# Kernel tuning notes

Measured on AMD Instinct MI355X. Metric: run time of the kernel, lower is better.

The kernel has to match this reference:

```python
import jax, jax.numpy as jnp
import numpy as np

N_NODES = 50000
N_EDGES = 1600000
IN_DIM = 128
HID = 128
N_GRAPHS = 64
N_CLASSES = 1


def _seg_sum(x, ids, n):
    return jax.ops.segment_sum(x, ids, num_segments=n)


def _gcn_layer(h, W, b, src, dst, src_isqrt, dst_isqrt):
    # DGL GraphConv, norm='both': D_dst^{-1/2} A D_src^{-1/2} (h W) + b
    hw = h @ W                                  # [N, out]
    msg = (hw * src_isqrt[:, None])[src]        # gather -> [E, out]
    agg = _seg_sum(msg, dst, h.shape[0])        # scatter-add -> [N, out]
    return agg * dst_isqrt[:, None] + b


def setup_inputs() -> dict:
    key = jax.random.key(0)
    ks = jax.random.split(key, 16)
    x = jax.random.normal(ks[0], (N_NODES, IN_DIM), dtype=jnp.float32)
    src = jax.random.randint(ks[1], (N_EDGES,), 0, N_NODES)
    dst = jax.random.randint(ks[2], (N_EDGES,), 0, N_NODES)
    graph_id = jnp.sort(jax.random.randint(ks[3], (N_NODES,), 0, N_GRAPHS))
    s = 1.0 / np.sqrt(HID)
    params = {
        'W1': jax.random.uniform(ks[4], (IN_DIM, HID), jnp.float32, -s, s),
        'b1': jnp.zeros((HID,), jnp.float32),
        'W2': jax.random.uniform(ks[5], (HID, HID), jnp.float32, -s, s),
        'b2': jnp.zeros((HID,), jnp.float32),
        'Wc1': jax.random.uniform(ks[6], (HID, HID // 2), jnp.float32, -s, s),
        'bc1': jnp.zeros((HID // 2,), jnp.float32),
        'Wc2': jax.random.uniform(ks[7], (HID // 2, HID // 4), jnp.float32, -s, s),
        'bc2': jnp.zeros((HID // 4,), jnp.float32),
        'Wc3': jax.random.uniform(ks[8], (HID // 4, HID // 8), jnp.float32, -s, s),
        'bc3': jnp.zeros((HID // 8,), jnp.float32),
        'Wc4': jax.random.uniform(ks[9], (HID // 8, N_CLASSES), jnp.float32, -s, s),
        'bc4': jnp.zeros((N_CLASSES,), jnp.float32),
    }
    return dict(x=x, src=src, dst=dst, graph_id=graph_id, num_graphs=N_GRAPHS, **params)


def reference(x, src, dst, graph_id, num_graphs, W1, b1, W2, b2,
              Wc1, bc1, Wc2, bc2, Wc3, bc3, Wc4, bc4):
    n = x.shape[0]
    ones = jnp.ones((src.shape[0],), x.dtype)
    out_deg = jnp.clip(_seg_sum(ones, src, n), 1.0)
    in_deg = jnp.clip(_seg_sum(ones, dst, n), 1.0)
    src_isqrt = jax.lax.rsqrt(out_deg)
    dst_isqrt = jax.lax.rsqrt(in_deg)

    h = jax.nn.relu(_gcn_layer(x, W1, b1, src, dst, src_isqrt, dst_isqrt))
    h = jax.nn.relu(_gcn_layer(h, W2, b2, src, dst, src_isqrt, dst_isqrt))

    # dgl.mean_nodes: per-graph mean of node features
    sums = _seg_sum(h, graph_id, num_graphs)                       # [G, HID]
    cnts = jnp.clip(_seg_sum(jnp.ones((n,), h.dtype), graph_id, num_graphs), 1.0)
    hg = sums / cnts[:, None]

    o = jax.nn.relu(hg @ Wc1 + bc1)
    o = jax.nn.relu(o @ Wc2 + bc2)
    o = jax.nn.relu(o @ Wc3 + bc3)
    return o @ Wc4 + bc4
```

## Files before the change

kernel.cpp:

```cpp
#include <hip/hip_runtime.h>
#include <hip/hip_fp16.h>

#define FDIM 128
#define NGRAPH 64
#define CBLK 256
#define OCH2 12800
#define OSL 64

typedef _Float16 f16;
typedef f16 f16x8 __attribute__((ext_vector_type(8)));
typedef float f32x4 __attribute__((ext_vector_type(4)));
typedef float f32x2 __attribute__((ext_vector_type(2)));

__device__ __forceinline__ int lower_bound_i(const int* a, int n, int v) {
    int lo = 0, hi = n;
    while (lo < hi) { int m = (lo + hi) >> 1; if (a[m] < v) lo = m + 1; else hi = m; }
    return lo;
}

__global__ __launch_bounds__(256) void k_pre(
        const float* __restrict__ W1, f16* __restrict__ W1h, f16* __restrict__ W1l,
        const float* __restrict__ W2, f16* __restrict__ W2h, f16* __restrict__ W2l,
        float* __restrict__ hg, const int* __restrict__ src, const int* __restrict__ dst,
        unsigned* __restrict__ od_part, int* __restrict__ partial,
        int E, int NBIN, int CE4, int NH) {
    __shared__ __align__(16) unsigned shmem_u[OCH2];
    const int t = threadIdx.x;
    int b = blockIdx.x;
    if (b < 128) {
        int i = b * 256 + t;
        if (i < NGRAPH * FDIM) hg[i] = 0.f;
        int j = i & 16383;
        int k = j >> 7, n = j & 127;
        const float* W = (i < 16384) ? W1 : W2;
        f16* Wh = (i < 16384) ? W1h : W2h;
        f16* Wl = (i < 16384) ? W1l : W2l;
        float v = W[j];
        f16 hi = (f16)v;
        Wh[n * FDIM + k] = hi;
        Wl[n * FDIM + k] = (f16)(v - (float)hi);
    } else if (b < 128 + CBLK) {
        b -= 128;
        int* lds = (int*)shmem_u;
        for (int i = t; i < 4 * 257; i += 256) lds[i] = 0;
        __syncthreads();
        const int wv = t >> 6;
        int* hh = &lds[wv * 257];
        const int s = b * CE4, e = min(E, s + CE4);
        for (int i = s + t * 4; i < e; i += 1024) {
            if (i + 4 <= e) {
                uint4 d4 = *(const uint4*)&dst[i];
                atomicAdd(&hh[d4.x >> 8], 1);
                atomicAdd(&hh[d4.y >> 8], 1);
                atomicAdd(&hh[d4.z >> 8], 1);
                atomicAdd(&hh[d4.w >> 8], 1);
            } else {
                for (int j = i; j < e; j++) atomicAdd(&hh[dst[j] >> 8], 1);
            }
        }
        __syncthreads();
        for (int i = t; i < NBIN; i += 256)
            partial[i * CBLK + b] = lds[i] + lds[257 + i] + lds[514 + i] + lds[771 + i];
    } else {
        const int ob = b - 128 - CBLK;
        const int c  = ob >> 6;
        const int sl = ob & (OSL - 1);
        for (int i = t; i < OCH2; i += 256) shmem_u[i] = 0u;
        __syncthreads();
        const int plo = c * OCH2;
        const int vlo = plo * 2;
        const int SE = (((E + OSL - 1) / OSL) + 3) & ~3;
        const int s = sl * SE, e = min(E, s + SE);
        for (int i = s + t * 4; i < e; i += 1024) {
            if (i + 4 <= e) {
                uint4 s4 = *(const uint4*)&src[i];
                int v0 = (int)s4.x - vlo, v1 = (int)s4.y - vlo;
                int v2 = (int)s4.z - vlo, v3 = (int)s4.w - vlo;
                if ((unsigned)v0 < (unsigned)(2 * OCH2))
                    atomicAdd(&shmem_u[v0 >> 1], 1u << ((v0 & 1) * 16));
                if ((unsigned)v1 < (unsigned)(2 * OCH2))
                    atomicAdd(&shmem_u[v1 >> 1], 1u << ((v1 & 1) * 16));
                if ((unsigned)v2 < (unsigned)(2 * OCH2))
                    atomicAdd(&shmem_u[v2 >> 1], 1u << ((v2 & 1) * 16));
                if ((unsigned)v3 < (unsigned)(2 * OCH2))
                    atomicAdd(&shmem_u[v3 >> 1], 1u << ((v3 & 1) * 16));
            } else {
                for (int j = i; j < e; j++) {
                    int v = src[j] - vlo;
                    if ((unsigned)v < (unsigned)(2 * OCH2))
                        atomicAdd(&shmem_u[v >> 1], 1u << ((v & 1) * 16));
                }
            }
        }
        __syncthreads();
        const int hiN = min(NH - plo, OCH2);
        for (int i = t; i < hiN; i += 256)
            od_part[(size_t)sl * NH + plo + i] = shmem_u[i];
    }
}

__global__ __launch_bounds__(256) void k_scan(
        const int* __restrict__ partial, int* __restrict__ offs, int* __restrict__ bsum,
        int M, const unsigned* __restrict__ od_part, float* __restrict__ sisq,
        int NH, int N, int NBIN) {
    __shared__ int lds[256];
    const int t = threadIdx.x;
    int b = blockIdx.x;
    if (b < NBIN) {
        int i = b * 256 + t;
        int v = (i < M) ? partial[i] : 0;
        lds[t] = v;
        __syncthreads();
        for (int off = 1; off < 256; off <<= 1) {
            int x = (t >= off) ? lds[t - off] : 0;
            __syncthreads();
            lds[t] += x;
            __syncthreads();
        }
        if (i < M) offs[i] = lds[t] - v;
        if (t == 255) bsum[b] = lds[t];
    } else {
        b -= NBIN;
        const int i = b * 256 + t;
        if (i < NH) {
            unsigned lo = 0, hi = 0;
#pragma unroll 8
            for (int s = 0; s < OSL; s++) {
                unsigned v = od_part[(size_t)s * NH + i];
                lo += v & 0xFFFFu;
                hi += v >> 16;
            }
            const int n0 = 2 * i, n1 = 2 * i + 1;
            sisq[n0] = rsqrtf((float)max((int)lo, 1));
            if (n1 < N) sisq[n1] = rsqrtf((float)max((int)hi, 1));
        }
    }
}

__global__ __launch_bounds__(256) void k_coarse_scatter(
        const int* __restrict__ src, const int* __restrict__ dst,
        const int* __restrict__ offs, const int* __restrict__ bsum,
        unsigned* __restrict__ coarse_buf, int E, int CE4, int NBIN) {
    __shared__ int cur[256], sb[256];
    const int t = threadIdx.x, b = blockIdx.x;
    int v = (t < NBIN) ? bsum[t] : 0;
    sb[t] = v;
    __syncthreads();
    for (int off = 1; off < 256; off <<= 1) {
        int x = (t >= off) ? sb[t - off] : 0;
        __syncthreads();
        sb[t] += x;
        __syncthreads();
    }
    if (t < NBIN) cur[t] = offs[t * CBLK + b] + (sb[t] - v);
    __syncthreads();
    const int s = b * CE4, e = min(E, s + CE4);
    for (int i = s + t * 4; i < e; i += 1024) {
        if (i + 4 <= e) {
            uint4 d4 = *(const uint4*)&dst[i];
            uint4 s4 = *(const uint4*)&src[i];
            int p0 = atomicAdd(&cur[d4.x >> 8], 1);
            int p1 = atomicAdd(&cur[d4.y >> 8], 1);
            int p2 = atomicAdd(&cur[d4.z >> 8], 1);
            int p3 = atomicAdd(&cur[d4.w >> 8], 1);
            coarse_buf[p0] = (d4.x << 16) | s4.x;
            coarse_buf[p1] = (d4.y << 16) | s4.y;
            coarse_buf[p2] = (d4.z << 16) | s4.z;
            coarse_buf[p3] = (d4.w << 16) | s4.w;
        } else {
            for (int j = i; j < e; j++) {
                unsigned d = (unsigned)dst[j];
                int p = atomicAdd(&cur[d >> 8], 1);
                coarse_buf[p] = (d << 16) | (unsigned)src[j];
            }
        }
    }
}

template<bool IN_F16>
__device__ __forceinline__ void gemm_body(
        f16* smem, float* sisql, int blk,
        const void* __restrict__ Xv, const f16* __restrict__ Wh,
        const f16* __restrict__ Wl, const float* __restrict__ sisq,
        unsigned char* __restrict__ out, int N) {
    const int t = threadIdx.x;
    const int w = t >> 6;
    const int lane = t & 63;
    const int base = blk * 128;

    if (t < 128) {
        int row = base + t;
        sisql[t] = (row < N) ? sisq[row] : 1.f;
    }
    for (int i = t; i < 2048; i += 256) {
        int n = i >> 4, kc = (i & 15) * 8;
        *(uint4*)&smem[n * 136 + kc] = *(const uint4*)&Wh[n * FDIM + kc];
    }
    __syncthreads();

    const int mrow = lane & 15;
    const int kq = (lane >> 4) * 8;
    const int arow0 = min(base + w * 32 + mrow, N - 1);
    const int arow1 = min(base + w * 32 + 16 + mrow, N - 1);

    f16x8 a0[4], a1[4];
    if (IN_F16) {
        const f16* X = (const f16*)Xv;
#pragma unroll
        for (int kk = 0; kk < 4; kk++) {
            a0[kk] = *(const f16x8*)&X[(size_t)arow0 * FDIM + kk * 32 + kq];
            a1[kk] = *(const f16x8*)&X[(size_t)arow1 * FDIM + kk * 32 + kq];
        }
    } else {
        const float* X = (const float*)Xv;
#pragma unroll
        for (int kk = 0; kk < 4; kk++) {
            float4 u0 = *(const float4*)&X[(size_t)arow0 * FDIM + kk * 32 + kq];
            float4 u1 = *(const float4*)&X[(size_t)arow0 * FDIM + kk * 32 + kq + 4];
            float4 v0 = *(const float4*)&X[(size_t)arow1 * FDIM + kk * 32 + kq];
            float4 v1 = *(const float4*)&X[(size_t)arow1 * FDIM + kk * 32 + kq + 4];
            f16x8 av;
            av[0] = (f16)u0.x; av[1] = (f16)u0.y; av[2] = (f16)u0.z; av[3] = (f16)u0.w;
            av[4] = (f16)u1.x; av[5] = (f16)u1.y; av[6] = (f16)u1.z; av[7] = (f16)u1.w;
            a0[kk] = av;
            av[0] = (f16)v0.x; av[1] = (f16)v0.y; av[2] = (f16)v0.z; av[3] = (f16)v0.w;
            av[4] = (f16)v1.x; av[5] = (f16)v1.y; av[6] = (f16)v1.z; av[7] = (f16)v1.w;
            a1[kk] = av;
        }
    }

    f32x4 acc0[8], acc1[8];
#pragma unroll
    for (int nt = 0; nt < 8; nt++) {
        acc0[nt] = (f32x4){0.f, 0.f, 0.f, 0.f};
        acc1[nt] = (f32x4){0.f, 0.f, 0.f, 0.f};
    }

#pragma unroll
    for (int kk = 0; kk < 4; kk++) {
#pragma unroll
        for (int nt = 0; nt < 8; nt++) {
            f16x8 bh = *(const f16x8*)&smem[(nt * 16 + mrow) * 136 + kk * 32 + kq];
            f16x8 bl = *(const f16x8*)&Wl[(nt * 16 + mrow) * FDIM + kk * 32 + kq];
            acc0[nt] = __builtin_amdgcn_mfma_f32_16x16x32_f16(a0[kk], bh, acc0[nt], 0, 0, 0);
            acc1[nt] = __builtin_amdgcn_mfma_f32_16x16x32_f16(a1[kk], bh, acc1[nt], 0, 0, 0);
            acc0[nt] = __builtin_amdgcn_mfma_f32_16x16x32_f16(a0[kk], bl, acc0[nt], 0, 0, 0);
            acc1[nt] = __builtin_amdgcn_mfma_f32_16x16x32_f16(a1[kk], bl, acc1[nt], 0, 0, 0);
        }
    }

    const int r0 = (lane >> 4) * 4;
    float sv0[4], sv1[4];
#pragma unroll
    for (int j = 0; j < 4; j++) {
        sv0[j] = sisql[w * 32 + r0 + j];
        sv1[j] = sisql[w * 32 + 16 + r0 + j];
    }
    __syncthreads();
#pragma unroll
    for (int nt = 0; nt < 8; nt++) {
        int c = nt * 16 + mrow;
#pragma unroll
        for (int j = 0; j < 4; j++) {
            smem[(w * 32 + r0 + j) * 136 + c]      = (f16)(acc0[nt][j] * sv0[j]);
            smem[(w * 32 + 16 + r0 + j) * 136 + c] = (f16)(acc1[nt][j] * sv1[j]);
        }
    }
    __syncthreads();
    {
        int r = t >> 1, cb = (t & 1) * 64;
        int row = base + r;
        if (row < N) {
            unsigned char* dstp = out + (size_t)row * FDIM + cb;
#pragma unroll
            for (int g2 = 0; g2 < 4; g2++) {
                unsigned wv[4];
#pragma unroll
                for (int k2 = 0; k2 < 4; k2++) {
                    const f16* p = &smem[r * 136 + cb + g2 * 16 + k2 * 4];
                    int w0 = __builtin_amdgcn_cvt_pk_fp8_f32((float)p[0], (float)p[1], 0, false);
                    w0 = __builtin_amdgcn_cvt_pk_fp8_f32((float)p[2], (float)p[3], w0, true);
                    wv[k2] = (unsigned)w0;
                }
                uint4 u;
                u.x = wv[0]; u.y = wv[1]; u.z = wv[2]; u.w = wv[3];
                *(uint4*)&dstp[g2 * 16] = u;
            }
        }
    }
}

__global__ __launch_bounds__(256) void k_fine_gemm(
        const unsigned* __restrict__ coarse_buf, const int* __restrict__ bsum,
        int* __restrict__ csr_src, int* __restrict__ row_ptr, int N, int E, int NBIN,
        const float* __restrict__ x, const f16* __restrict__ Wh,
        const f16* __restrict__ Wl, const float* __restrict__ sisq,
        unsigned char* __restrict__ hws) {
    __shared__ __align__(16) f16 smem[128 * 136];
    __shared__ float sisql[128];
    const int t = threadIdx.x;
    const int g = blockIdx.x;
    if (g >= NBIN) {
        gemm_body<false>(smem, sisql, g - NBIN, x, Wh, Wl, sisq, hws, N);
        return;
    }
    int* h  = (int*)smem;
    int* sc = h + 256;
    int* cur = h + 512;
    int bv = (t < NBIN) ? bsum[t] : 0;
    sc[t] = bv;
    __syncthreads();
    for (int off = 1; off < 256; off <<= 1) {
        int xx = (t >= off) ? sc[t - off] : 0;
        __syncthreads();
        sc[t] += xx;
        __syncthreads();
    }
    __syncthreads();
    if (t == 0) { h[0] = sc[g] - bsum[g]; h[1] = sc[g]; }
    __syncthreads();
    const int s = h[0], e = h[1];
    __syncthreads();
    h[t] = 0;
    __syncthreads();
    for (int i = s + t; i < e; i += 256)
        atomicAdd(&h[(coarse_buf[i] >> 16) & 255], 1);
    __syncthreads();
    int v = h[t];
    sc[t] = v;
    __syncthreads();
    for (int off = 1; off < 256; off <<= 1) {
        int xx = (t >= off) ? sc[t - off] : 0;
        __syncthreads();
        sc[t] += xx;
        __syncthreads();
    }
    const int excl = sc[t] - v;
    const int node = g * 256 + t;
    if (node < N) row_ptr[node] = s + excl;
    if (node == N) row_ptr[N] = s + excl;
    cur[t] = s + excl;
    __syncthreads();
    for (int i = s + t; i < e; i += 256) {
        unsigned p = coarse_buf[i];
        int f = (p >> 16) & 255;
        int pos = atomicAdd(&cur[f], 1);
        csr_src[pos] = (int)(p & 0xFFFFu);
    }
    if (g == NBIN - 1 && t == 0 && (N & 255) == 0) row_ptr[N] = E;
}

__global__ __launch_bounds__(256) void k_gemm2(
        const f16* __restrict__ X, const f16* __restrict__ Wh,
        const f16* __restrict__ Wl, const float* __restrict__ sisq,
        unsigned char* __restrict__ out, int N) {
    __shared__ __align__(16) f16 smem[128 * 136];
    __shared__ float sisql[128];
    gemm_body<true>(smem, sisql, blockIdx.x, X, Wh, Wl, sisq, out, N);
}

__device__ __forceinline__ void accF8(float* acc, uint2 v) {
    f32x2 a0 = __builtin_amdgcn_cvt_pk_f32_fp8((int)v.x, false);
    f32x2 a1 = __builtin_amdgcn_cvt_pk_f32_fp8((int)v.x, true);
    f32x2 a2 = __builtin_amdgcn_cvt_pk_f32_fp8((int)v.y, false);
    f32x2 a3 = __builtin_amdgcn_cvt_pk_f32_fp8((int)v.y, true);
    acc[0] += a0.x; acc[1] += a0.y; acc[2] += a1.x; acc[3] += a1.y;
    acc[4] += a2.x; acc[5] += a2.y; acc[6] += a3.x; acc[7] += a3.y;
}

template<bool POOL>
__global__ __launch_bounds__(256) void k_aggregate(
        const unsigned char* __restrict__ hws, const int* __restrict__ csr_src,
        const int* __restrict__ row_ptr,
        const float* __restrict__ bias, f16* __restrict__ out,
        const int* __restrict__ gid, float* __restrict__ hg, int N) {
    const int t = threadIdx.x;
    const int node = blockIdx.x * 8 + (t >> 5);
    const int ln = t & 31;
    const int half = ln >> 4;
    const int fbase = (ln & 15) * 8;

    int s = 0, e = 0;
    if (node < N) { s = row_ptr[node]; e = row_ptr[node + 1]; }
    const int len = e - s;
    const int mid = s + ((len + 1) >> 1);
    int i  = half ? mid : s;
    const int en = half ? e : mid;

    float acc[8];
#pragma unroll
    for (int j = 0; j < 8; j++) acc[j] = 0.f;

    for (; i + 8 <= en; i += 8) {
        int u[8];
#pragma unroll
        for (int j = 0; j < 8; j++) u[j] = csr_src[i + j];
        uint2 v[8];
#pragma unroll
        for (int j = 0; j < 8; j++)
            v[j] = *(const uint2*)(hws + (size_t)u[j] * FDIM + fbase);
#pragma unroll
        for (int j = 0; j < 8; j++) accF8(acc, v[j]);
    }
    if (i + 4 <= en) {
        int u[4];
#pragma unroll
        for (int j = 0; j < 4; j++) u[j] = csr_src[i + j];
        uint2 v[4];
#pragma unroll
        for (int j = 0; j < 4; j++)
            v[j] = *(const uint2*)(hws + (size_t)u[j] * FDIM + fbase);
#pragma unroll
        for (int j = 0; j < 4; j++) accF8(acc, v[j]);
        i += 4;
    }
    for (; i < en; i++) {
        int u = csr_src[i];
        uint2 v = *(const uint2*)(hws + (size_t)u * FDIM + fbase);
        accF8(acc, v);
    }

#pragma unroll
    for (int j = 0; j < 8; j++) acc[j] += __shfl_xor(acc[j], 16, 64);

    const float d = rsqrtf((float)max(len, 1));
    float res[8];
#pragma unroll
    for (int j = 0; j < 8; j++)
        res[j] = fmaxf(fmaf(acc[j], d, bias[fbase + j]), 0.f);

    if (!POOL) {
        if (node < N && half == 0) {
            f16 r16[8];
#pragma unroll
            for (int j = 0; j < 8; j++) r16[j] = (f16)res[j];
            *(uint4*)(out + (size_t)node * FDIM + fbase) = *(const uint4*)r16;
        }
    } else {
        __shared__ float hgl[8 * 128];
        const int nfirst = blockIdx.x * 8;
        const int nlast = min(nfirst + 7, N - 1);
        const int g0 = gid[nfirst];
        const int span = gid[nlast] - g0 + 1;
        if (span <= 8) {
            for (int k = t; k < span * 128; k += 256) hgl[k] = 0.f;
            __syncthreads();
            if (node < N && half == 0) {
                const int gg = gid[node] - g0;
#pragma unroll
                for (int j = 0; j < 8; j++)
                    atomicAdd(&hgl[gg * 128 + fbase + j], res[j]);
            }
            __syncthreads();
            for (int k = t; k < span * 128; k += 256)
                atomicAdd(&hg[g0 * 128 + k], hgl[k]);
        } else {
            if (node < N && half == 0) {
                const int gg = gid[node];
#pragma unroll
                for (int j = 0; j < 8; j++)
                    atomicAdd(&hg[gg * 128 + fbase + j], res[j]);
            }
        }
    }
}

__global__ __launch_bounds__(256) void k_mlp(
        const float* __restrict__ hg, const int* __restrict__ gid, int N,
        const float* __restrict__ Wc1, const float* __restrict__ bc1,
        const float* __restrict__ Wc2, const float* __restrict__ bc2,
        const float* __restrict__ Wc3, const float* __restrict__ bc3,
        const float* __restrict__ Wc4, const float* __restrict__ bc4,
        float* __restrict__ out) {
    __shared__ float A[NGRAPH * 128];
    __shared__ float O1[NGRAPH * 64];
    __shared__ float O2[NGRAPH * 32];
    __shared__ float O3[NGRAPH * 16];
    __shared__ float inv_cnt[NGRAPH];
    const int t = threadIdx.x;

    if (t < NGRAPH) {
        int s = lower_bound_i(gid, N, t);
        int e = lower_bound_i(gid, N, t + 1);
        inv_cnt[t] = 1.f / fmaxf((float)(e - s), 1.f);
    }
    __syncthreads();

    for (int i = t; i < NGRAPH * 128; i += 256) A[i] = hg[i] * inv_cnt[i >> 7];
    __syncthreads();

    for (int i = t; i < NGRAPH * 64; i += 256) {
        int g = i >> 6, o = i & 63;
        float a = bc1[o];
        for (int k = 0; k < 128; k++) a = fmaf(A[g * 128 + k], Wc1[k * 64 + o], a);
        O1[i] = fmaxf(a, 0.f);
    }
    __syncthreads();

    for (int i = t; i < NGRAPH * 32; i += 256) {
        int g = i >> 5, o = i & 31;
        float a = bc2[o];
        for (int k = 0; k < 64; k++) a = fmaf(O1[g * 64 + k], Wc2[k * 32 + o], a);
        O2[i] = fmaxf(a, 0.f);
    }
    __syncthreads();

    for (int i = t; i < NGRAPH * 16; i += 256) {
        int g = i >> 4, o = i & 15;
        float a = bc3[o];
        for (int k = 0; k < 32; k++) a = fmaf(O2[g * 32 + k], Wc3[k * 16 + o], a);
        O3[i] = fmaxf(a, 0.f);
    }
    __syncthreads();

    if (t < NGRAPH) {
        float a = bc4[0];
        for (int k = 0; k < 16; k++) a = fmaf(O3[t * 16 + k], Wc4[k], a);
        out[t] = a;
    }
}

extern "C" void kernel_launch(void* const* d_in, const int* in_sizes, int n_in,
                              void* d_out, int out_size, void* d_ws, size_t ws_size,
                              hipStream_t stream) {
    const float* x   = (const float*)d_in[0];
    const int*   src = (const int*)d_in[1];
    const int*   dst = (const int*)d_in[2];
    const int*   gid = (const int*)d_in[3];
    const float* W1  = (const float*)d_in[5];
    const float* b1  = (const float*)d_in[6];
    const float* W2  = (const float*)d_in[7];
    const float* b2  = (const float*)d_in[8];
    const float* Wc1 = (const float*)d_in[9];
    const float* bc1 = (const float*)d_in[10];
    const float* Wc2 = (const float*)d_in[11];
    const float* bc2 = (const float*)d_in[12];
    const float* Wc3 = (const float*)d_in[13];
    const float* bc3 = (const float*)d_in[14];
    const float* Wc4 = (const float*)d_in[15];
    const float* bc4 = (const float*)d_in[16];
    float* out = (float*)d_out;

    const int N = in_sizes[0] / FDIM;
    const int E = in_sizes[1];

    const int NBIN = (N + 255) >> 8;
    const int M    = NBIN * CBLK;
    const int CE4  = (((E + CBLK - 1) / CBLK) + 3) & ~3;
    const int NH   = (N + 1) >> 1;
    const int OC2  = (NH + OCH2 - 1) / OCH2;
    const int MB   = (NH + 255) >> 8;

    char* w = (char*)d_ws;
    size_t off = 0;
    auto alloc = [&](size_t bytes) -> void* {
        void* p = w + off;
        off = (off + bytes + 255) & ~(size_t)255;
        return p;
    };
    unsigned char* hws = (unsigned char*)alloc((size_t)N * FDIM);
    f16*   h       = (f16*)   alloc((size_t)N * FDIM * 2);
    int*   csr_src = (int*)   alloc((size_t)E * 4);
    unsigned* coarse_buf = (unsigned*)alloc((size_t)E * 4);
    unsigned* od_part = (unsigned*)alloc((size_t)OSL * NH * 4);
    int*   partial = (int*)   alloc((size_t)M * 4);
    int*   offs    = (int*)   alloc((size_t)M * 4);
    int*   row_ptr = (int*)   alloc((size_t)(N + 1) * 4);
    float* sisq    = (float*) alloc((size_t)N * 4);
    int*   bsum    = (int*)   alloc(256 * 4);
    float* hg      = (float*) alloc(NGRAPH * FDIM * 4);
    f16*   W1t     = (f16*)   alloc(FDIM * FDIM * 2);
    f16*   W1l     = (f16*)   alloc(FDIM * FDIM * 2);
    f16*   W2t     = (f16*)   alloc(FDIM * FDIM * 2);
    f16*   W2l     = (f16*)   alloc(FDIM * FDIM * 2);

    const int gT = (N + 127) / 128;
    const int gA = (N + 7) / 8;

    k_pre<<<128 + CBLK + OC2 * OSL, 256, 0, stream>>>(
        W1, W1t, W1l, W2, W2t, W2l, hg, src, dst, od_part, partial, E, NBIN, CE4, NH);
    k_scan<<<NBIN + MB, 256, 0, stream>>>(partial, offs, bsum, M, od_part, sisq, NH, N, NBIN);
    k_coarse_scatter<<<CBLK, 256, 0, stream>>>(src, dst, offs, bsum, coarse_buf, E, CE4, NBIN);
    k_fine_gemm<<<NBIN + gT, 256, 0, stream>>>(
        coarse_buf, bsum, csr_src, row_ptr, N, E, NBIN,
        x, W1t, W1l, sisq, hws);
    k_aggregate<false><<<gA, 256, 0, stream>>>(hws, csr_src, row_ptr, b1, h, nullptr, nullptr, N);
    k_gemm2<<<gT, 256, 0, stream>>>(h, W2t, W2l, sisq, hws, N);
    k_aggregate<true><<<gA, 256, 0, stream>>>(hws, csr_src, row_ptr, b2, nullptr, gid, hg, N);
    k_mlp<<<1, 256, 0, stream>>>(hg, gid, N, Wc1, bc1, Wc2, bc2, Wc3, bc3, Wc4, bc4, out);
}
```

Before: 285.4 us.

## Stage CSR scatters in LDS and store 16-bit source indices

The coarse scatter now sorts each block's edges into a local LDS buffer, using per-block bin histograms, before writing contiguous runs to the global coarse buffer. The fine pass likewise builds each bin's CSR segment in LDS and then writes it out coalesced, with a direct-write fallback for oversized bins. csr_src shrinks from int to unsigned short, which halves index traffic in both aggregation passes. This relies on node ids fitting in 16 bits and on a block's edges fitting in the fixed-size LDS stage, and the larger LDS footprint may lower occupancy.

```diff
diff --git a/kernel.cpp b/kernel.cpp
--- a/kernel.cpp
+++ b/kernel.cpp
@@ -6,6 +6,7 @@
 #define CBLK 256
 #define OCH2 12800
 #define OSL 64
+#define FSTAGE 12288
 
 typedef _Float16 f16;
 typedef f16 f16x8 __attribute__((ext_vector_type(8)));
@@ -140,19 +141,33 @@
 __global__ __launch_bounds__(256) void k_coarse_scatter(
         const int* __restrict__ src, const int* __restrict__ dst,
         const int* __restrict__ offs, const int* __restrict__ bsum,
+        const int* __restrict__ partial,
         unsigned* __restrict__ coarse_buf, int E, int CE4, int NBIN) {
-    __shared__ int cur[256], sb[256];
+    __shared__ int G[256], lo[256], cur[256], sc[256];
+    __shared__ unsigned stage[6272];
     const int t = threadIdx.x, b = blockIdx.x;
     int v = (t < NBIN) ? bsum[t] : 0;
-    sb[t] = v;
+    sc[t] = v;
     __syncthreads();
     for (int off = 1; off < 256; off <<= 1) {
-        int x = (t >= off) ? sb[t - off] : 0;
-        __syncthreads();
-        sb[t] += x;
-        __syncthreads();
-    }
-    if (t < NBIN) cur[t] = offs[t * CBLK + b] + (sb[t] - v);
+        int x = (t >= off) ? sc[t - off] : 0;
+        __syncthreads();
+        sc[t] += x;
+        __syncthreads();
+    }
+    if (t < NBIN) G[t] = offs[t * CBLK + b] + (sc[t] - v);
+    __syncthreads();
+    int hv = (t < NBIN) ? partial[t * CBLK + b] : 0;
+    sc[t] = hv;
+    __syncthreads();
+    for (int off = 1; off < 256; off <<= 1) {
+        int x = (t >= off) ? sc[t - off] : 0;
+        __syncthreads();
+        sc[t] += x;
+        __syncthreads();
+    }
+    lo[t] = sc[t] - hv;
+    cur[t] = sc[t] - hv;
     __syncthreads();
     const int s = b * CE4, e = min(E, s + CE4);
     for (int i = s + t * 4; i < e; i += 1024) {
@@ -163,17 +178,24 @@
             int p1 = atomicAdd(&cur[d4.y >> 8], 1);
             int p2 = atomicAdd(&cur[d4.z >> 8], 1);
             int p3 = atomicAdd(&cur[d4.w >> 8], 1);
-            coarse_buf[p0] = (d4.x << 16) | s4.x;
-            coarse_buf[p1] = (d4.y << 16) | s4.y;
-            coarse_buf[p2] = (d4.z << 16) | s4.z;
-            coarse_buf[p3] = (d4.w << 16) | s4.w;
+            stage[p0] = (d4.x << 16) | s4.x;
+            stage[p1] = (d4.y << 16) | s4.y;
+            stage[p2] = (d4.z << 16) | s4.z;
+            stage[p3] = (d4.w << 16) | s4.w;
         } else {
             for (int j = i; j < e; j++) {
                 unsigned d = (unsigned)dst[j];
                 int p = atomicAdd(&cur[d >> 8], 1);
-                coarse_buf[p] = (d << 16) | (unsigned)src[j];
+                stage[p] = (d << 16) | (unsigned)src[j];
             }
         }
+    }
+    __syncthreads();
+    const int nloc = e - s;
+    for (int i = t; i < nloc; i += 256) {
+        unsigned p = stage[i];
+        int f = p >> 24;
+        coarse_buf[G[f] + (i - lo[f])] = p;
     }
 }
 
@@ -292,7 +314,8 @@
 
 __global__ __launch_bounds__(256) void k_fine_gemm(
         const unsigned* __restrict__ coarse_buf, const int* __restrict__ bsum,
-        int* __restrict__ csr_src, int* __restrict__ row_ptr, int N, int E, int NBIN,
+        unsigned short* __restrict__ csr_src, int* __restrict__ row_ptr,
+        int N, int E, int NBIN,
         const float* __restrict__ x, const f16* __restrict__ Wh,
         const f16* __restrict__ Wl, const float* __restrict__ sisq,
         unsigned char* __restrict__ hws) {
@@ -304,9 +327,11 @@
         gemm_body<false>(smem, sisql, g - NBIN, x, Wh, Wl, sisq, hws, N);
         return;
     }
-    int* h  = (int*)smem;
-    int* sc = h + 256;
+    int* h   = (int*)smem;
+    int* sc  = h + 256;
     int* cur = h + 512;
+    int* lo  = h + 768;
+    unsigned short* stage = (unsigned short*)(h + 1024);
     int bv = (t < NBIN) ? bsum[t] : 0;
     sc[t] = bv;
     __syncthreads();
@@ -316,10 +341,9 @@
         sc[t] += xx;
         __syncthreads();
     }
-    __syncthreads();
-    if (t == 0) { h[0] = sc[g] - bsum[g]; h[1] = sc[g]; }
-    __syncthreads();
-    const int s = h[0], e = h[1];
+    if (t == 0) { cur[0] = sc[g] - bsum[g]; cur[1] = sc[g]; }
+    __syncthreads();
+    const int s = cur[0], e = cur[1];
     __syncthreads();
     h[t] = 0;
     __syncthreads();
@@ -339,13 +363,27 @@
     const int node = g * 256 + t;
     if (node < N) row_ptr[node] = s + excl;
     if (node == N) row_ptr[N] = s + excl;
-    cur[t] = s + excl;
-    __syncthreads();
-    for (int i = s + t; i < e; i += 256) {
-        unsigned p = coarse_buf[i];
-        int f = (p >> 16) & 255;
-        int pos = atomicAdd(&cur[f], 1);
-        csr_src[pos] = (int)(p & 0xFFFFu);
+    lo[t] = excl;
+    cur[t] = excl;
+    __syncthreads();
+    const int len = e - s;
+    if (len <= FSTAGE) {
+        for (int i = s + t; i < e; i += 256) {
+            unsigned p = coarse_buf[i];
+            int f = (p >> 16) & 255;
+            int pos = atomicAdd(&cur[f], 1);
+            stage[pos] = (unsigned short)(p & 0xFFFFu);
+        }
+        __syncthreads();
+        for (int i = t; i < len; i += 256)
+            csr_src[s + i] = stage[i];
+    } else {
+        for (int i = s + t; i < e; i += 256) {
+            unsigned p = coarse_buf[i];
+            int f = (p >> 16) & 255;
+            int pos = atomicAdd(&cur[f], 1);
+            csr_src[s + pos] = (unsigned short)(p & 0xFFFFu);
+        }
     }
     if (g == NBIN - 1 && t == 0 && (N & 255) == 0) row_ptr[N] = E;
 }
@@ -370,7 +408,8 @@
 
 template<bool POOL>
 __global__ __launch_bounds__(256) void k_aggregate(
-        const unsigned char* __restrict__ hws, const int* __restrict__ csr_src,
+        const unsigned char* __restrict__ hws,
+        const unsigned short* __restrict__ csr_src,
         const int* __restrict__ row_ptr,
         const float* __restrict__ bias, f16* __restrict__ out,
         const int* __restrict__ gid, float* __restrict__ hg, int N) {
@@ -560,7 +599,7 @@
     };
     unsigned char* hws = (unsigned char*)alloc((size_t)N * FDIM);
     f16*   h       = (f16*)   alloc((size_t)N * FDIM * 2);
-    int*   csr_src = (int*)   alloc((size_t)E * 4);
+    unsigned short* csr_src = (unsigned short*)alloc((size_t)E * 2);
     unsigned* coarse_buf = (unsigned*)alloc((size_t)E * 4);
     unsigned* od_part = (unsigned*)alloc((size_t)OSL * NH * 4);
     int*   partial = (int*)   alloc((size_t)M * 4);
@@ -580,7 +619,8 @@
     k_pre<<<128 + CBLK + OC2 * OSL, 256, 0, stream>>>(
         W1, W1t, W1l, W2, W2t, W2l, hg, src, dst, od_part, partial, E, NBIN, CE4, NH);
     k_scan<<<NBIN + MB, 256, 0, stream>>>(partial, offs, bsum, M, od_part, sisq, NH, N, NBIN);
-    k_coarse_scatter<<<CBLK, 256, 0, stream>>>(src, dst, offs, bsum, coarse_buf, E, CE4, NBIN);
+    k_coarse_scatter<<<CBLK, 256, 0, stream>>>(
+        src, dst, offs, bsum, partial, coarse_buf, E, CE4, NBIN);
     k_fine_gemm<<<NBIN + gT, 256, 0, stream>>>(
         coarse_buf, bsum, csr_src, row_ptr, N, E, NBIN,
         x, W1t, W1l, sisq, hws);
```

Measured after the change: 277.6 us. 2.7% less time.
